# Kernel tuning notes

Hardware: AMD Instinct MI355X
Metric: run time of the kernel (lower is better)

## Reference

```python
import jax, jax.numpy as jnp
import numpy as np

V = 50000   # input_size == output_size (one-hot vocab)
H = 256     # hidden_size
B = 512     # batch_size
L = 1       # num_layers

def setup_inputs() -> dict:
    key = jax.random.key(0)
    ks = jax.random.split(key, 9)
    s = 1.0 / np.sqrt(H)  # torch default uniform(-1/sqrt(H), 1/sqrt(H))
    inp = {
        "input": jax.random.randint(ks[0], (B,), 0, V, dtype=jnp.int64 if jax.config.jax_enable_x64 else jnp.int32),
        "target": jax.random.randint(ks[1], (B,), 0, V, dtype=jnp.int64 if jax.config.jax_enable_x64 else jnp.int32),
        "hidden": jax.random.normal(ks[2], (L, B, H), dtype=jnp.float32),
        "w_ih": jax.random.uniform(ks[3], (3 * H, V), jnp.float32, -s, s),
        "w_hh": jax.random.uniform(ks[4], (3 * H, H), jnp.float32, -s, s),
        "b_ih": jax.random.uniform(ks[5], (3 * H,), jnp.float32, -s, s),
        "b_hh": jax.random.uniform(ks[6], (3 * H,), jnp.float32, -s, s),
        "w_out": jax.random.uniform(ks[7], (V, H), jnp.float32, -s, s),
        "b_out": jax.random.uniform(ks[8], (V,), jnp.float32, -s, s),
    }
    return inp

def reference(input, target, hidden, w_ih, w_hh, b_ih, b_hh, w_out, b_out):
    # one-hot(input) @ w_ih.T is exactly a row-gather from w_ih.T  -> (B, 3H)
    h0 = hidden[0]                              # (B, H), num_layers == 1
    x_proj = w_ih.T[input] + b_ih               # (B, 3H)
    h_proj = h0 @ w_hh.T + b_hh                 # (B, 3H)
    xr, xz, xn = jnp.split(x_proj, 3, axis=-1)
    hr, hz, hn = jnp.split(h_proj, 3, axis=-1)
    r = jax.nn.sigmoid(xr + hr)                 # reset gate
    z = jax.nn.sigmoid(xz + hz)                 # update gate
    n = jnp.tanh(xn + r * hn)                   # candidate
    h1 = (1.0 - z) * n + z * h0                 # (B, H)
    logit = jnp.tanh(h1 @ w_out.T + b_out)      # (B, V)
    return logit, h1[None]                      # (B,V), (1,B,H)
```

## Files before the change

### kernel.cpp

```cpp
#include <hip/hip_runtime.h>
#include <hip/hip_bf16.h>

#define VOCAB 50000
#define HID   256
#define BATCH 512
#define GH    768

typedef __attribute__((ext_vector_type(8))) __bf16 bf16x8;
typedef __attribute__((ext_vector_type(4))) float f32x4;
typedef __attribute__((ext_vector_type(4))) unsigned int u32x4;

union BFrag {
    bf16x8 v;
    u32x4  q;
    __bf16 b[8];
};

__device__ __forceinline__ float fast_sigmoid(float x) {
    return 1.0f / (1.0f + __expf(-x));
}
__device__ __forceinline__ float fast_tanh(float x) {
    return 1.0f - 2.0f / (1.0f + __expf(2.0f * x));
}

__device__ __forceinline__ void cvt8(BFrag& t, f32x4 lo, f32x4 hi) {
    t.b[0] = (__bf16)lo.x; t.b[1] = (__bf16)lo.y;
    t.b[2] = (__bf16)lo.z; t.b[3] = (__bf16)lo.w;
    t.b[4] = (__bf16)hi.x; t.b[5] = (__bf16)hi.y;
    t.b[6] = (__bf16)hi.z; t.b[7] = (__bf16)hi.w;
}

__global__ __launch_bounds__(256, 4) void gemm_swp(
    const unsigned short* __restrict__ Abf, const float* __restrict__ Bm,
    float* __restrict__ C, const float* __restrict__ bias, int mChunks)
{
    __shared__ char ldsA[2][16384];

    const int tid  = threadIdx.x;
    const int wid  = tid >> 6;
    const int lane = tid & 63;
    const int r    = lane & 15;
    const int g    = lane >> 4;
    const int wcol = blockIdx.x * 64 + wid * 16 + r;
    const int bw   = wcol < VOCAB ? wcol : (VOCAB - 1);

    BFrag bf[8];
    {
        const f32x4* wrow = reinterpret_cast<const f32x4*>(Bm + (size_t)bw * 256);
        #pragma unroll
        for (int kk = 0; kk < 8; kk++) {
            f32x4 lo = __builtin_nontemporal_load(&wrow[kk * 8 + g * 2]);
            f32x4 hi = __builtin_nontemporal_load(&wrow[kk * 8 + g * 2 + 1]);
            cvt8(bf[kk], lo, hi);
        }
    }
    #pragma unroll
    for (int kk = 0; kk < 8; kk++)
        asm volatile("" : "+v"(bf[kk].q));

    const int vcol0   = blockIdx.x * 64 + wid * 16 + g * 4;
    const bool storeok = (vcol0 + 3 < VOCAB);
    const int bvc     = storeok ? vcol0 : (VOCAB - 4);
    const f32x4 b4    = *reinterpret_cast<const f32x4*>(bias + bvc);

    u32x4 areg[4];
    auto load_chunk = [&](int c) {
        const u32x4* src = reinterpret_cast<const u32x4*>(Abf + (size_t)c * 32 * 256);
        #pragma unroll
        for (int i = 0; i < 4; i++) areg[i] = src[tid + i * 256];
    };
    auto write_lds = [&](int buf) {
        #pragma unroll
        for (int i = 0; i < 4; i++) {
            int u = tid + i * 256;
            int row = u >> 5, j = u & 31;
            int byte = row * 512 + ((j ^ (row & 7)) << 4);
            *reinterpret_cast<u32x4*>(&ldsA[buf][byte]) = areg[i];
        }
    };

    load_chunk(0);
    write_lds(0);
    if (mChunks > 1) load_chunk(1);
    asm volatile("s_waitcnt lgkmcnt(0)\n\ts_barrier" ::: "memory");

    for (int c = 0; c < mChunks; c++) {
        const int cur = c & 1;
        if (c + 1 < mChunks) {
            write_lds(cur ^ 1);
            if (c + 2 < mChunks) load_chunk(c + 2);
        }

        f32x4 acc0 = (f32x4){0.f, 0.f, 0.f, 0.f};
        f32x4 acc1 = (f32x4){0.f, 0.f, 0.f, 0.f};

        #pragma unroll
        for (int kk = 0; kk < 8; kk++) {
            const int s0 = r * 512 + ((((kk << 2) + g) ^ (r & 7)) << 4);
            BFrag a0, a1;
            a0.q = *reinterpret_cast<const u32x4*>(&ldsA[cur][s0]);
            a1.q = *reinterpret_cast<const u32x4*>(&ldsA[cur][s0 + 8192]);
            acc0 = __builtin_amdgcn_mfma_f32_16x16x32_bf16(bf[kk].v, a0.v, acc0, 0, 0, 0);
            acc1 = __builtin_amdgcn_mfma_f32_16x16x32_bf16(bf[kk].v, a1.v, acc1, 0, 0, 0);
        }

        if (storeok) {
            const int row0 = c * 32 + r;
            f32x4 v0, v1;
            #pragma unroll
            for (int j = 0; j < 4; j++) {
                v0[j] = fast_tanh(acc0[j] + b4[j]);
                v1[j] = fast_tanh(acc1[j] + b4[j]);
            }
            *reinterpret_cast<f32x4*>(&C[(size_t)row0 * VOCAB + vcol0])        = v0;
            *reinterpret_cast<f32x4*>(&C[(size_t)(row0 + 16) * VOCAB + vcol0]) = v1;
        }

        if (c + 1 < mChunks)
            asm volatile("s_waitcnt lgkmcnt(0)\n\ts_barrier" ::: "memory");
    }
}

__global__ __launch_bounds__(256, 4) void gemm_h(
    const float* __restrict__ A, const float* __restrict__ Bm,
    float* __restrict__ C)
{
    __shared__ char ldsA[16384];

    const int tid  = threadIdx.x;
    const int wid  = tid >> 6;
    const int lane = tid & 63;
    const int r    = lane & 15;
    const int g    = lane >> 4;
    const int col  = blockIdx.x * 64 + wid * 16 + r;
    const int mbase = blockIdx.y * 32;

    BFrag bf[8];
    {
        const f32x4* wrow = reinterpret_cast<const f32x4*>(Bm + (size_t)col * 256);
        #pragma unroll
        for (int kk = 0; kk < 8; kk++)
            cvt8(bf[kk], wrow[kk * 8 + g * 2], wrow[kk * 8 + g * 2 + 1]);
    }

    {
        const f32x4* src = reinterpret_cast<const f32x4*>(A + (size_t)mbase * 256);
        #pragma unroll
        for (int i = 0; i < 4; i++) {
            int u = tid + i * 256;
            int row = u >> 5, jj = u & 31;
            BFrag t; cvt8(t, src[2 * u], src[2 * u + 1]);
            int byte = row * 512 + ((jj ^ (row & 7)) << 4);
            *reinterpret_cast<u32x4*>(&ldsA[byte]) = t.q;
        }
    }
    __syncthreads();

    f32x4 acc0 = (f32x4){0.f, 0.f, 0.f, 0.f};
    f32x4 acc1 = (f32x4){0.f, 0.f, 0.f, 0.f};
    #pragma unroll
    for (int kk = 0; kk < 8; kk++) {
        const int s0 = r * 512 + ((((kk << 2) + g) ^ (r & 7)) << 4);
        BFrag a0, a1;
        a0.q = *reinterpret_cast<const u32x4*>(&ldsA[s0]);
        a1.q = *reinterpret_cast<const u32x4*>(&ldsA[s0 + 8192]);
        acc0 = __builtin_amdgcn_mfma_f32_16x16x32_bf16(a0.v, bf[kk].v, acc0, 0, 0, 0);
        acc1 = __builtin_amdgcn_mfma_f32_16x16x32_bf16(a1.v, bf[kk].v, acc1, 0, 0, 0);
    }

    const int rowb = mbase + g * 4;
    #pragma unroll
    for (int j = 0; j < 4; j++) {
        C[(size_t)(rowb + j) * GH + col]      = acc0[j];
        C[(size_t)(rowb + 16 + j) * GH + col] = acc1[j];
    }
}

__global__ __launch_bounds__(256) void gru_gate(
    const int* __restrict__ inp, const float* __restrict__ hidden,
    const float* __restrict__ w_ih, const float* __restrict__ b_ih,
    const float* __restrict__ b_hh, const float* __restrict__ hproj,
    float* __restrict__ h1out, unsigned short* __restrict__ h1bf)
{
    const int b = blockIdx.x;
    const int k = threadIdx.x;
    const int c = inp[b];

    float xr = w_ih[(size_t)k * VOCAB + c]         + b_ih[k];
    float xz = w_ih[(size_t)(k + 256) * VOCAB + c] + b_ih[k + 256];
    float xn = w_ih[(size_t)(k + 512) * VOCAB + c] + b_ih[k + 512];

    float hr = hproj[b * GH + k]       + b_hh[k];
    float hz = hproj[b * GH + 256 + k] + b_hh[k + 256];
    float hn = hproj[b * GH + 512 + k] + b_hh[k + 512];

    float rg = fast_sigmoid(xr + hr);
    float zg = fast_sigmoid(xz + hz);
    float ng = fast_tanh(xn + rg * hn);
    float h0 = hidden[b * HID + k];
    float h1 = (1.0f - zg) * ng + zg * h0;

    h1out[b * HID + k] = h1;
    __bf16 hb = (__bf16)h1;
    h1bf[b * HID + k] = __builtin_bit_cast(unsigned short, hb);
}

extern "C" void kernel_launch(void* const* d_in, const int* in_sizes, int n_in,
                              void* d_out, int out_size, void* d_ws, size_t ws_size,
                              hipStream_t stream) {
    const int*   input  = (const int*)  d_in[0];
    const float* hidden = (const float*)d_in[2];
    const float* w_ih   = (const float*)d_in[3];
    const float* w_hh   = (const float*)d_in[4];
    const float* b_ih   = (const float*)d_in[5];
    const float* b_hh   = (const float*)d_in[6];
    const float* w_out  = (const float*)d_in[7];
    const float* b_out  = (const float*)d_in[8];

    float* logit = (float*)d_out;
    float* h1    = (float*)d_out + (size_t)BATCH * VOCAB;

    float*          hproj = (float*)d_ws;
    unsigned short* h1bf  = (unsigned short*)((char*)d_ws + (size_t)BATCH * GH * 4);

    dim3 g1(GH / 64, BATCH / 32);
    gemm_h<<<g1, 256, 0, stream>>>(hidden, w_hh, hproj);

    gru_gate<<<BATCH, 256, 0, stream>>>(input, hidden, w_ih, b_ih, b_hh, hproj,
                                        h1, h1bf);

    dim3 g3((VOCAB + 63) / 64, 1);
    gemm_swp<<<g3, 256, 0, stream>>>(h1bf, w_out, logit, b_out, 16);
}
```

Measured before the change: 67.48 us.

## Switch output GEMM to 32x32x16 MFMA with 64-row chunks and single LDS buffer

Rewrites the vocabulary projection kernel to use 32x32x16 bf16 MFMA instructions. Each wave now holds 32 columns of w_out in registers and processes 32 batch rows, with the block taking 64-row chunks over 8 iterations instead of 32-row chunks over 16. The double-buffered LDS scheme is replaced by one larger buffer with explicit barriers before and after each write, and occupancy is lowered to 3 blocks. The aim is higher MFMA throughput and fewer loop iterations, at the cost of more registers and less overlap between LDS writes and compute.

After: 101.1 us. +49.8%, slower.

```diff
diff --git a/kernel.cpp b/kernel.cpp
--- a/kernel.cpp
+++ b/kernel.cpp
@@ -6,9 +6,10 @@
 #define BATCH 512
 #define GH    768
 
-typedef __attribute__((ext_vector_type(8))) __bf16 bf16x8;
-typedef __attribute__((ext_vector_type(4))) float f32x4;
-typedef __attribute__((ext_vector_type(4))) unsigned int u32x4;
+typedef __attribute__((ext_vector_type(8)))  __bf16 bf16x8;
+typedef __attribute__((ext_vector_type(4)))  float  f32x4;
+typedef __attribute__((ext_vector_type(16))) float  f32x16;
+typedef __attribute__((ext_vector_type(4)))  unsigned int u32x4;
 
 union BFrag {
     bf16x8 v;
@@ -30,94 +31,99 @@
     t.b[6] = (__bf16)hi.z; t.b[7] = (__bf16)hi.w;
 }
 
-__global__ __launch_bounds__(256, 4) void gemm_swp(
+__global__ __launch_bounds__(256, 3) void gemm_swp32(
     const unsigned short* __restrict__ Abf, const float* __restrict__ Bm,
     float* __restrict__ C, const float* __restrict__ bias, int mChunks)
 {
-    __shared__ char ldsA[2][16384];
+    __shared__ char ldsA[64 * 512];
 
     const int tid  = threadIdx.x;
     const int wid  = tid >> 6;
     const int lane = tid & 63;
-    const int r    = lane & 15;
-    const int g    = lane >> 4;
-    const int wcol = blockIdx.x * 64 + wid * 16 + r;
-    const int bw   = wcol < VOCAB ? wcol : (VOCAB - 1);
-
-    BFrag bf[8];
+    const int cl   = lane & 31;
+    const int h    = lane >> 5;
+    const int wc   = wid & 1;
+    const int wr   = wid >> 1;
+
+    const int colwave = blockIdx.x * 64 + wc * 32;
+    const int wcol    = colwave + cl;
+    const int bw      = wcol < VOCAB ? wcol : (VOCAB - 1);
+
+    BFrag bf[16];
     {
         const f32x4* wrow = reinterpret_cast<const f32x4*>(Bm + (size_t)bw * 256);
         #pragma unroll
-        for (int kk = 0; kk < 8; kk++) {
-            f32x4 lo = __builtin_nontemporal_load(&wrow[kk * 8 + g * 2]);
-            f32x4 hi = __builtin_nontemporal_load(&wrow[kk * 8 + g * 2 + 1]);
-            cvt8(bf[kk], lo, hi);
-        }
-    }
-    #pragma unroll
-    for (int kk = 0; kk < 8; kk++)
-        asm volatile("" : "+v"(bf[kk].q));
-
-    const int vcol0   = blockIdx.x * 64 + wid * 16 + g * 4;
-    const bool storeok = (vcol0 + 3 < VOCAB);
-    const int bvc     = storeok ? vcol0 : (VOCAB - 4);
-    const f32x4 b4    = *reinterpret_cast<const f32x4*>(bias + bvc);
-
-    u32x4 areg[4];
+        for (int ks = 0; ks < 16; ks++) {
+            f32x4 lo = __builtin_nontemporal_load(&wrow[ks * 4 + h * 2]);
+            f32x4 hi = __builtin_nontemporal_load(&wrow[ks * 4 + h * 2 + 1]);
+            cvt8(bf[ks], lo, hi);
+        }
+    }
+    #pragma unroll
+    for (int ks = 0; ks < 16; ks++)
+        asm volatile("" : "+v"(bf[ks].q));
+
+    f32x4 b4[4];
+    #pragma unroll
+    for (int q = 0; q < 4; q++) {
+        int c0 = colwave + 8 * q + 4 * h;
+        if (c0 + 4 > VOCAB) c0 = VOCAB - 4;
+        b4[q] = *reinterpret_cast<const f32x4*>(bias + c0);
+    }
+
+    u32x4 areg[8];
     auto load_chunk = [&](int c) {
-        const u32x4* src = reinterpret_cast<const u32x4*>(Abf + (size_t)c * 32 * 256);
-        #pragma unroll
-        for (int i = 0; i < 4; i++) areg[i] = src[tid + i * 256];
+        const u32x4* src = reinterpret_cast<const u32x4*>(Abf + (size_t)c * 64 * 256);
+        #pragma unroll
+        for (int i = 0; i < 8; i++) areg[i] = src[tid + i * 256];
     };
-    auto write_lds = [&](int buf) {
-        #pragma unroll
-        for (int i = 0; i < 4; i++) {
+    auto write_lds = [&]() {
+        #pragma unroll
+        for (int i = 0; i < 8; i++) {
             int u = tid + i * 256;
             int row = u >> 5, j = u & 31;
             int byte = row * 512 + ((j ^ (row & 7)) << 4);
-            *reinterpret_cast<u32x4*>(&ldsA[buf][byte]) = areg[i];
+            *reinterpret_cast<u32x4*>(&ldsA[byte]) = areg[i];
         }
     };
 
     load_chunk(0);
-    write_lds(0);
-    if (mChunks > 1) load_chunk(1);
-    asm volatile("s_waitcnt lgkmcnt(0)\n\ts_barrier" ::: "memory");
 
     for (int c = 0; c < mChunks; c++) {
-        const int cur = c & 1;
-        if (c + 1 < mChunks) {
-            write_lds(cur ^ 1);
-            if (c + 2 < mChunks) load_chunk(c + 2);
-        }
-
-        f32x4 acc0 = (f32x4){0.f, 0.f, 0.f, 0.f};
-        f32x4 acc1 = (f32x4){0.f, 0.f, 0.f, 0.f};
-
-        #pragma unroll
-        for (int kk = 0; kk < 8; kk++) {
-            const int s0 = r * 512 + ((((kk << 2) + g) ^ (r & 7)) << 4);
-            BFrag a0, a1;
-            a0.q = *reinterpret_cast<const u32x4*>(&ldsA[cur][s0]);
-            a1.q = *reinterpret_cast<const u32x4*>(&ldsA[cur][s0 + 8192]);
-            acc0 = __builtin_amdgcn_mfma_f32_16x16x32_bf16(bf[kk].v, a0.v, acc0, 0, 0, 0);
-            acc1 = __builtin_amdgcn_mfma_f32_16x16x32_bf16(bf[kk].v, a1.v, acc1, 0, 0, 0);
-        }
-
-        if (storeok) {
-            const int row0 = c * 32 + r;
-            f32x4 v0, v1;
-            #pragma unroll
-            for (int j = 0; j < 4; j++) {
-                v0[j] = fast_tanh(acc0[j] + b4[j]);
-                v1[j] = fast_tanh(acc1[j] + b4[j]);
+        if (c > 0)
+            asm volatile("s_barrier" ::: "memory");
+
+        write_lds();
+        asm volatile("s_waitcnt lgkmcnt(0)\n\ts_barrier" ::: "memory");
+
+        if (c + 1 < mChunks) load_chunk(c + 1);
+
+        f32x16 acc;
+        #pragma unroll
+        for (int i = 0; i < 16; i++) acc[i] = 0.0f;
+
+        const int lrow = wr * 32 + cl;
+        #pragma unroll
+        for (int ks = 0; ks < 16; ks++) {
+            const int jj = ks * 2 + h;
+            const int byte = lrow * 512 + ((jj ^ (lrow & 7)) << 4);
+            BFrag hb;
+            hb.q = *reinterpret_cast<const u32x4*>(&ldsA[byte]);
+            acc = __builtin_amdgcn_mfma_f32_32x32x16_bf16(bf[ks].v, hb.v, acc, 0, 0, 0);
+        }
+
+        const int grow = c * 64 + wr * 32 + cl;
+        #pragma unroll
+        for (int q = 0; q < 4; q++) {
+            const int col0 = colwave + 8 * q + 4 * h;
+            if (col0 + 4 <= VOCAB) {
+                f32x4 v;
+                #pragma unroll
+                for (int j = 0; j < 4; j++)
+                    v[j] = fast_tanh(acc[q * 4 + j] + b4[q][j]);
+                *reinterpret_cast<f32x4*>(&C[(size_t)grow * VOCAB + col0]) = v;
             }
-            *reinterpret_cast<f32x4*>(&C[(size_t)row0 * VOCAB + vcol0])        = v0;
-            *reinterpret_cast<f32x4*>(&C[(size_t)(row0 + 16) * VOCAB + vcol0]) = v1;
-        }
-
-        if (c + 1 < mChunks)
-            asm volatile("s_waitcnt lgkmcnt(0)\n\ts_barrier" ::: "memory");
+        }
     }
 }
 
@@ -230,5 +236,5 @@
                                         h1, h1bf);
 
     dim3 g3((VOCAB + 63) / 64, 1);
-    gemm_swp<<<g3, 256, 0, stream>>>(h1bf, w_out, logit, b_out, 16);
-}
+    gemm_swp32<<<g3, 256, 0, stream>>>(h1bf, w_out, logit, b_out, 8);
+}
```
